# Kernel optimization log

Hardware: AMD Instinct MI355X
Metric: run time of the kernel (lower is better)

The kernel has to match this reference:

```python
import jax, jax.numpy as jnp
import numpy as np

N = 3072        # nodes
F_IN = 512      # input_dim
F_OUT = 256     # output_dim
ORDER = 2       # Cayley polynomial order
JACOBI = 3      # Jacobi fixed-point iterations per order


def setup_inputs() -> dict:
    key = jax.random.key(0)
    k1, k2, k3, k4, k5 = jax.random.split(key, 5)
    # normalized-adjacency-like matrix: row sums ~1 so h*Laplacian is well scaled
    adj = jax.random.uniform(k1, (N, N), dtype=jnp.float32) * (2.0 / N)
    x = jax.random.normal(k2, (N, F_IN), dtype=jnp.float32)
    h = jnp.float32(1.0)  # spectral zoom parameter
    w0 = jax.random.normal(k3, (F_IN, F_OUT), dtype=jnp.float32) * 0.05
    wr = jax.random.normal(k4, (ORDER, F_IN, F_OUT), dtype=jnp.float32) * 0.05
    wi = jax.random.normal(k5, (ORDER, F_IN, F_OUT), dtype=jnp.float32) * 0.05
    return {"x": x, "adj": adj, "h": h, "w0": w0, "wr": wr, "wi": wi}


def _cayley_forward(x, adj, h, w0, wr, wi):
    c64 = jnp.complex64
    j1 = jnp.asarray(1j, dtype=c64)
    n = adj.shape[0]
    I = jnp.eye(n, dtype=jnp.float32)
    # h * Laplacian, L = I - A_norm  (complex64, as in the TF code)
    hL = (h * (I - adj)).astype(c64)
    # Jacobi diagonal: rowsum(hL) + i  (constant across iterations)
    diag_inv = 1.0 / (jnp.sum(hL, axis=1) + j1)  # [n]

    # support[0] = I  ->  real part of I @ (x @ w0) is just x @ w0
    out = x @ w0  # [n, F_OUT] float32

    xc = x.astype(c64)
    csum = jnp.zeros((n, w0.shape[1]), dtype=c64)
    prev = I.astype(c64)
    for j in range(ORDER):
        # rhs of the linear system: x_j = hL @ prev - i*prev
        xj = hL @ prev - j1 * prev
        # Jacobi iterations: y <- y + D^{-1} (x_j - (hL @ y + i*y))
        y = xj
        for _ in range(JACOBI):
            y = y + diag_inv[:, None] * (xj - (hL @ y + j1 * y))
        W = jax.lax.complex(wr[j], wi[j])          # [F_IN, F_OUT] complex64
        csum = csum + y @ (xc @ W)                  # support_j @ pre_sup
        prev = y
    out = out + 2.0 * jnp.real(csum).astype(jnp.float32)
    return jax.nn.relu(out)


def reference(x, adj, h, w0, wr, wi):
    return _cayley_forward(x, adj, h, w0, wr, wi)
```

## Files before the change

kernel.cpp:

```cpp
#include <hip/hip_runtime.h>
#include <hip/hip_bf16.h>

#define NN 3072
#define FIN 512
#define FOUT 256

typedef __attribute__((ext_vector_type(8))) short short8;
typedef __attribute__((ext_vector_type(4))) float f32x4;

__device__ __forceinline__ short f2bf(float f) {
  union { float f; unsigned u; } v; v.f = f;
  unsigned r = v.u + 0x7fffu + ((v.u >> 16) & 1u);
  return (short)(r >> 16);
}

__device__ __forceinline__ void glds16(const short* g, short* l) {
  __builtin_amdgcn_global_load_lds(
      (const __attribute__((address_space(1))) unsigned*)g,
      (__attribute__((address_space(3))) unsigned*)l, 16, 0, 0);
}

template<int N> __device__ __forceinline__ void wait_vm() {
  if constexpr (N == 0) asm volatile("s_waitcnt vmcnt(0)" ::: "memory");
  else                  asm volatile("s_waitcnt vmcnt(4)" ::: "memory");
}


__global__ __launch_bounds__(256) void prep_adj(const float* __restrict__ adj,
    short* __restrict__ adjbf, float2* __restrict__ dinv, const float* __restrict__ hptr)
{
  int m = blockIdx.x;
  int tid = threadIdx.x;
  const float4* row = (const float4*)(adj + (size_t)m * NN);
  short4* obf = (short4*)(adjbf + (size_t)m * NN);
  float sum = 0.f;
#pragma unroll
  for (int i = 0; i < NN / 4 / 256; ++i) {
    int idx = i * 256 + tid;
    float4 v = row[idx];
    sum += (v.x + v.y) + (v.z + v.w);
    obf[idx] = make_short4(f2bf(v.x), f2bf(v.y), f2bf(v.z), f2bf(v.w));
  }
#pragma unroll
  for (int off = 32; off > 0; off >>= 1) sum += __shfl_down(sum, off, 64);
  __shared__ float red[4];
  if ((tid & 63) == 0) red[tid >> 6] = sum;
  __syncthreads();
  if (tid == 0) {
    float s = red[0] + red[1] + red[2] + red[3];
    float h = hptr[0];
    float r = h * (1.f - s);
    float den = r * r + 1.f;
    dinv[m] = make_float2(r / den, -1.f / den);
  }
}

__global__ __launch_bounds__(256) void prep_x(const float* __restrict__ x, short* __restrict__ xbf) {
  int idx = blockIdx.x * 256 + threadIdx.x;
  float4 v = ((const float4*)x)[idx];
  ((short4*)xbf)[idx] = make_short4(f2bf(v.x), f2bf(v.y), f2bf(v.z), f2bf(v.w));
}

__global__ __launch_bounds__(256) void prep_w(const float* __restrict__ w0,
    const float* __restrict__ wr, const float* __restrict__ wi, short* __restrict__ wpack)
{
  int idx = blockIdx.x * 256 + threadIdx.x;
  int f = idx & 511;
  int i = idx >> 9;
  float v;
  if (i < 1024) {
    int j = (i < 512) ? 1 : 0;
    int local = i & 511;
    int c = local >> 1;
    const float* src = (local & 1) ? wi : wr;
    v = src[((size_t)j * FIN + f) * FOUT + c];
  } else {
    v = w0[(size_t)f * FOUT + (i - 1024)];
  }
  wpack[idx] = f2bf(v);
}

template<int MODE, int KTOT, int ITILES>
__global__ __launch_bounds__(256, 4) void gemm_t(
    const short* __restrict__ Apan, int lda,
    const short* __restrict__ Badj, int ldb,
    const float* __restrict__ Vin,
    const float* __restrict__ Yin,
    float* __restrict__ Fout,
    short* __restrict__ Bout,
    const float2* __restrict__ dinv,
    const float* __restrict__ hptr)
{
  constexpr int BK = 64;
  constexpr int NT = KTOT / BK;

  __shared__ short As[2][64 * BK];
  __shared__ short Bs[2][64 * BK];

  const int tid  = threadIdx.x;
  const int lane = tid & 63;
  const int w    = tid >> 6;
  const int l15  = lane & 15;
  const int wrow = w >> 1, wcol = w & 1;

  const int bid = blockIdx.x;
  const int xcd = bid & 7;
  const int s   = bid >> 3;
  const int jt  = xcd * 6 + s / ITILES;
  const int it  = s % ITILES;

  const int i0 = it * 64;
  const int j0 = jt * 64;

  const int srow = lane >> 3;
  const int scol = ((lane & 7) ^ srow) * 8;

  const short* aSrc = Apan + (size_t)i0 * lda;
  const short* bSrc = Badj + (size_t)j0 * ldb;

  auto STAGE = [&](int t) {
    const int k0 = t * BK;
    short* at = As[t & 1];
    short* bt = Bs[t & 1];
#pragma unroll
    for (int li = 0; li < 2; ++li) {
      int rb = (w * 2 + li) * 8;
      glds16(aSrc + (size_t)(rb + srow) * lda + k0 + scol, at + rb * BK);
    }
#pragma unroll
    for (int li = 0; li < 2; ++li) {
      int rb = (w * 2 + li) * 8;
      glds16(bSrc + (size_t)(rb + srow) * ldb + k0 + scol, bt + rb * BK);
    }
  };

  f32x4 acc[2][2];
#pragma unroll
  for (int a = 0; a < 2; a++)
#pragma unroll
    for (int b = 0; b < 2; b++) acc[a][b] = (f32x4){0.f, 0.f, 0.f, 0.f};

  STAGE(0);
  STAGE(1);

  for (int t = 0; t < NT; ++t) {
    if (t < NT - 1) wait_vm<4>(); else wait_vm<0>();
    __builtin_amdgcn_s_barrier();
    asm volatile("" ::: "memory");

    const short* at = As[t & 1];
    const short* bt = Bs[t & 1];
#pragma unroll
    for (int kk = 0; kk < 2; ++kk) {
      const int cb = kk * 4 + (lane >> 4);
      short8 af[2], bfr[2];
#pragma unroll
      for (int a = 0; a < 2; ++a) {
        int ra = wrow * 32 + a * 16 + l15;
        int c = cb ^ (ra & 7);
        af[a] = *(const short8*)(at + ra * BK + c * 8);
      }
#pragma unroll
      for (int b = 0; b < 2; ++b) {
        int rb = wcol * 32 + b * 16 + l15;
        int c = cb ^ (rb & 7);
        bfr[b] = *(const short8*)(bt + rb * BK + c * 8);
      }
      __builtin_amdgcn_s_setprio(1);
#pragma unroll
      for (int a = 0; a < 2; ++a)
#pragma unroll
        for (int b = 0; b < 2; ++b)
          acc[a][b] = __builtin_amdgcn_mfma_f32_16x16x32_bf16(af[a], bfr[b], acc[a][b], 0, 0, 0);
      __builtin_amdgcn_s_setprio(0);
    }

    asm volatile("" ::: "memory");
    __builtin_amdgcn_s_barrier();
    asm volatile("" ::: "memory");
    if (t + 2 < NT) STAGE(t + 2);
  }

  const float hv = hptr[0];
  const int ibase = i0 + wrow * 32 + ((lane >> 4) << 2);
#pragma unroll
  for (int a = 0; a < 2; ++a) {
    const int ia = ibase + a * 16;
#pragma unroll
    for (int b = 0; b < 2; ++b) {
      const int jb = j0 + wcol * 32 + b * 16 + l15;
      f32x4 c = acc[a][b];
      if (MODE == 0) {
#pragma unroll
        for (int q = 0; q < 4; ++q) {
          size_t off = (size_t)(ia + q) * NN + jb;
          Fout[off] = c[q];
          if (ia + q < 1024) Bout[off] = f2bf(c[q]);
        }
      } else if (MODE == 1) {
#pragma unroll
        for (int p = 0; p < 4; p += 2) {
          size_t offr = (size_t)(ia + p) * NN + jb;
          size_t offi = offr + NN;
          float vr = Vin[offr], vi = Vin[offi];
          float outr = hv * (vr - c[p])     + vi;
          float outi = hv * (vi - c[p + 1]) - vr;
          Fout[offr] = outr; Fout[offi] = outi;
          Bout[offr] = f2bf(outr); Bout[offi] = f2bf(outi);
        }
      } else {
#pragma unroll
        for (int p = 0; p < 4; p += 2) {
          size_t offr = (size_t)(ia + p) * NN + jb;
          size_t offi = offr + NN;
          float2 dv = dinv[jb];
          float vr = Vin[offr], vi = Vin[offi];
          float yr = Yin[offr], yi = Yin[offi];
          float tr_ = hv * (yr - c[p])     - yi;
          float ti_ = hv * (yi - c[p + 1]) + yr;
          float er = vr - tr_, ei = vi - ti_;
          float nyr = yr + dv.x * er - dv.y * ei;
          float nyi = yi + dv.x * ei + dv.y * er;
          Fout[offr] = nyr; Fout[offi] = nyi;
          Bout[offr] = f2bf(nyr); Bout[offi] = f2bf(nyi);
        }
      }
    }
  }
}

__global__ __launch_bounds__(256) void final_out(
    const float* __restrict__ Vbuf,
    const float* __restrict__ ybuf,
    float* __restrict__ out)
{
  __shared__ float t[64][65];
  int n0 = blockIdx.x * 64;
  int c0 = blockIdx.y * 64;
  int lane = threadIdx.x & 63;
  int wv = threadIdx.x >> 6;
#pragma unroll
  for (int s = 0; s < 16; s++) {
    int c = c0 + wv + s * 4;
    float o0 = Vbuf[(size_t)(1024 + c) * NN + n0 + lane];
    float u  = ybuf[(size_t)(2 * c) * NN + n0 + lane];
    float sv = ybuf[(size_t)(512 + 2 * c) * NN + n0 + lane];
    float v = o0 + 2.f * (u + sv);
    t[lane][wv + s * 4] = v > 0.f ? v : 0.f;
  }
  __syncthreads();
#pragma unroll
  for (int s = 0; s < 16; s++) {
    int nl = wv + s * 4;
    out[(size_t)(n0 + nl) * FOUT + c0 + lane] = t[nl][lane];
  }
}

extern "C" void kernel_launch(void* const* d_in, const int* in_sizes, int n_in,
                              void* d_out, int out_size, void* d_ws, size_t ws_size,
                              hipStream_t stream) {
  const float* x   = (const float*)d_in[0];
  const float* adj = (const float*)d_in[1];
  const float* h   = (const float*)d_in[2];
  const float* w0  = (const float*)d_in[3];
  const float* wr  = (const float*)d_in[4];
  const float* wi  = (const float*)d_in[5];
  float* out = (float*)d_out;

  char* ws = (char*)d_ws;
  size_t off = 0;
  auto alloc = [&](size_t bytes) {
    char* p = ws + off;
    off += (bytes + 255) & ~(size_t)255;
    return p;
  };
  short*  adjbf = (short*)alloc((size_t)NN * NN * 2);
  short*  xbf   = (short*)alloc((size_t)NN * FIN * 2);
  short*  wpack = (short*)alloc((size_t)1280 * FIN * 2);
  float2* dinv  = (float2*)alloc((size_t)NN * sizeof(float2));
  float*  Vbuf  = (float*)alloc((size_t)1280 * NN * 4);
  float*  ybuf  = (float*)alloc((size_t)1024 * NN * 4);
  short*  b0    = (short*)alloc((size_t)1024 * NN * 2);
  short*  b1    = (short*)alloc((size_t)1024 * NN * 2);

  prep_adj<<<NN, 256, 0, stream>>>(adj, adjbf, dinv, h);
  prep_x<<<(NN * FIN / 4) / 256, 256, 0, stream>>>(x, xbf);
  prep_w<<<(1280 * FIN) / 256, 256, 0, stream>>>(w0, wr, wi, wpack);

  gemm_t<0, FIN, 20><<<dim3(48 * 20), 256, 0, stream>>>(
      wpack, FIN, xbf, FIN, nullptr, nullptr, Vbuf, b0, dinv, h);
  gemm_t<1, NN, 16><<<dim3(48 * 16), 256, 0, stream>>>(
      b0, NN, adjbf, NN, Vbuf, nullptr, Vbuf, b1, dinv, h);
  gemm_t<2, NN, 16><<<dim3(48 * 16), 256, 0, stream>>>(
      b1, NN, adjbf, NN, Vbuf, Vbuf, ybuf, b0, dinv, h);
  gemm_t<2, NN, 16><<<dim3(48 * 16), 256, 0, stream>>>(
      b0, NN, adjbf, NN, Vbuf, ybuf, ybuf, b1, dinv, h);
  gemm_t<2, NN, 16><<<dim3(48 * 16), 256, 0, stream>>>(
      b1, NN, adjbf, NN, Vbuf, ybuf, ybuf, b0, dinv, h);
  gemm_t<1, NN, 8><<<dim3(48 * 8), 256, 0, stream>>>(
      b0, NN, adjbf, NN, ybuf, nullptr, Vbuf, b1, dinv, h);
  gemm_t<2, NN, 8><<<dim3(48 * 8), 256, 0, stream>>>(
      b1, NN, adjbf, NN, Vbuf, Vbuf, ybuf, b0, dinv, h);
  gemm_t<2, NN, 8><<<dim3(48 * 8), 256, 0, stream>>>(
      b0, NN, adjbf, NN, Vbuf, ybuf, ybuf, b1, dinv, h);
  gemm_t<2, NN, 8><<<dim3(48 * 8), 256, 0, stream>>>(
      b1, NN, adjbf, NN, Vbuf, ybuf, ybuf, b0, dinv, h);

  final_out<<<dim3(48, 4), 256, 0, stream>>>(Vbuf, ybuf, out);
}
```

Measured before the change: 381.9 us.

## Apply Horner-style nesting to share one propagation chain across both orders

Rewrites the two-order Cayley sum so that the order-1 and order-2 contributions flow through a single chain of adjacency products acting on 512 columns, instead of 1024 columns for the first four GEMMs. The last Jacobi step of the first stage adds the order-1 projected features (a new MODE 3 epilogue), and the second stage then carries the combined sum. This roughly halves the N-dimension width of the first four big GEMMs. It also merges the x and w conversion kernels into one launch. It relies on linearity of the Jacobi iterations, and the bf16 rounding now happens along a different path.

```diff
diff --git a/kernel.cpp b/kernel.cpp
--- a/kernel.cpp
+++ b/kernel.cpp
@@ -55,29 +55,31 @@
   }
 }
 
-__global__ __launch_bounds__(256) void prep_x(const float* __restrict__ x, short* __restrict__ xbf) {
-  int idx = blockIdx.x * 256 + threadIdx.x;
-  float4 v = ((const float4*)x)[idx];
-  ((short4*)xbf)[idx] = make_short4(f2bf(v.x), f2bf(v.y), f2bf(v.z), f2bf(v.w));
-}
-
-__global__ __launch_bounds__(256) void prep_w(const float* __restrict__ w0,
-    const float* __restrict__ wr, const float* __restrict__ wi, short* __restrict__ wpack)
+__global__ __launch_bounds__(256) void prep_xw(const float* __restrict__ x,
+    const float* __restrict__ w0, const float* __restrict__ wr,
+    const float* __restrict__ wi, short* __restrict__ xbf, short* __restrict__ wpack)
 {
-  int idx = blockIdx.x * 256 + threadIdx.x;
-  int f = idx & 511;
-  int i = idx >> 9;
-  float v;
-  if (i < 1024) {
-    int j = (i < 512) ? 1 : 0;
-    int local = i & 511;
-    int c = local >> 1;
-    const float* src = (local & 1) ? wi : wr;
-    v = src[((size_t)j * FIN + f) * FOUT + c];
+  int b = blockIdx.x;
+  if (b < 1536) {
+    int idx = b * 256 + threadIdx.x;
+    float4 v = ((const float4*)x)[idx];
+    ((short4*)xbf)[idx] = make_short4(f2bf(v.x), f2bf(v.y), f2bf(v.z), f2bf(v.w));
   } else {
-    v = w0[(size_t)f * FOUT + (i - 1024)];
-  }
-  wpack[idx] = f2bf(v);
+    int idx = (b - 1536) * 256 + threadIdx.x;
+    int f = idx & 511;
+    int i = idx >> 9;
+    float v;
+    if (i < 1024) {
+      int j = (i < 512) ? 1 : 0;
+      int local = i & 511;
+      int c = local >> 1;
+      const float* src = (local & 1) ? wi : wr;
+      v = src[((size_t)j * FIN + f) * FOUT + c];
+    } else {
+      v = w0[(size_t)f * FOUT + (i - 1024)];
+    }
+    wpack[idx] = f2bf(v);
+  }
 }
 
 template<int MODE, int KTOT, int ITILES>
@@ -86,6 +88,7 @@
     const short* __restrict__ Badj, int ldb,
     const float* __restrict__ Vin,
     const float* __restrict__ Yin,
+    const float* __restrict__ Min,
     float* __restrict__ Fout,
     short* __restrict__ Bout,
     const float2* __restrict__ dinv,
@@ -221,6 +224,10 @@
           float er = vr - tr_, ei = vi - ti_;
           float nyr = yr + dv.x * er - dv.y * ei;
           float nyi = yi + dv.x * ei + dv.y * er;
+          if (MODE == 3) {
+            nyr += Min[offr];
+            nyi += Min[offi];
+          }
           Fout[offr] = nyr; Fout[offi] = nyi;
           Bout[offr] = f2bf(nyr); Bout[offi] = f2bf(nyi);
         }
@@ -244,8 +251,7 @@
     int c = c0 + wv + s * 4;
     float o0 = Vbuf[(size_t)(1024 + c) * NN + n0 + lane];
     float u  = ybuf[(size_t)(2 * c) * NN + n0 + lane];
-    float sv = ybuf[(size_t)(512 + 2 * c) * NN + n0 + lane];
-    float v = o0 + 2.f * (u + sv);
+    float v = o0 + 2.f * u;
     t[lane][wv + s * 4] = v > 0.f ? v : 0.f;
   }
   __syncthreads();
@@ -279,32 +285,37 @@
   short*  wpack = (short*)alloc((size_t)1280 * FIN * 2);
   float2* dinv  = (float2*)alloc((size_t)NN * sizeof(float2));
   float*  Vbuf  = (float*)alloc((size_t)1280 * NN * 4);
-  float*  ybuf  = (float*)alloc((size_t)1024 * NN * 4);
+  float*  xjbuf = (float*)alloc((size_t)512 * NN * 4);
+  float*  ybuf  = (float*)alloc((size_t)512 * NN * 4);
   short*  b0    = (short*)alloc((size_t)1024 * NN * 2);
-  short*  b1    = (short*)alloc((size_t)1024 * NN * 2);
+  short*  b1    = (short*)alloc((size_t)512 * NN * 2);
+  short*  b2    = (short*)alloc((size_t)512 * NN * 2);
 
   prep_adj<<<NN, 256, 0, stream>>>(adj, adjbf, dinv, h);
-  prep_x<<<(NN * FIN / 4) / 256, 256, 0, stream>>>(x, xbf);
-  prep_w<<<(1280 * FIN) / 256, 256, 0, stream>>>(w0, wr, wi, wpack);
+  prep_xw<<<4096, 256, 0, stream>>>(x, w0, wr, wi, xbf, wpack);
+
+  const float* Q0f = Vbuf + (size_t)512 * NN;
 
   gemm_t<0, FIN, 20><<<dim3(48 * 20), 256, 0, stream>>>(
-      wpack, FIN, xbf, FIN, nullptr, nullptr, Vbuf, b0, dinv, h);
-  gemm_t<1, NN, 16><<<dim3(48 * 16), 256, 0, stream>>>(
-      b0, NN, adjbf, NN, Vbuf, nullptr, Vbuf, b1, dinv, h);
-  gemm_t<2, NN, 16><<<dim3(48 * 16), 256, 0, stream>>>(
-      b1, NN, adjbf, NN, Vbuf, Vbuf, ybuf, b0, dinv, h);
-  gemm_t<2, NN, 16><<<dim3(48 * 16), 256, 0, stream>>>(
-      b0, NN, adjbf, NN, Vbuf, ybuf, ybuf, b1, dinv, h);
-  gemm_t<2, NN, 16><<<dim3(48 * 16), 256, 0, stream>>>(
-      b1, NN, adjbf, NN, Vbuf, ybuf, ybuf, b0, dinv, h);
+      wpack, FIN, xbf, FIN, nullptr, nullptr, nullptr, Vbuf, b0, dinv, h);
+
   gemm_t<1, NN, 8><<<dim3(48 * 8), 256, 0, stream>>>(
-      b0, NN, adjbf, NN, ybuf, nullptr, Vbuf, b1, dinv, h);
-  gemm_t<2, NN, 8><<<dim3(48 * 8), 256, 0, stream>>>(
-      b1, NN, adjbf, NN, Vbuf, Vbuf, ybuf, b0, dinv, h);
-  gemm_t<2, NN, 8><<<dim3(48 * 8), 256, 0, stream>>>(
-      b0, NN, adjbf, NN, Vbuf, ybuf, ybuf, b1, dinv, h);
-  gemm_t<2, NN, 8><<<dim3(48 * 8), 256, 0, stream>>>(
-      b1, NN, adjbf, NN, Vbuf, ybuf, ybuf, b0, dinv, h);
+      b0, NN, adjbf, NN, Vbuf, nullptr, nullptr, xjbuf, b1, dinv, h);
+  gemm_t<2, NN, 8><<<dim3(48 * 8), 256, 0, stream>>>(
+      b1, NN, adjbf, NN, xjbuf, xjbuf, nullptr, ybuf, b2, dinv, h);
+  gemm_t<2, NN, 8><<<dim3(48 * 8), 256, 0, stream>>>(
+      b2, NN, adjbf, NN, xjbuf, ybuf, nullptr, ybuf, b1, dinv, h);
+  gemm_t<3, NN, 8><<<dim3(48 * 8), 256, 0, stream>>>(
+      b1, NN, adjbf, NN, xjbuf, ybuf, Q0f, xjbuf, b2, dinv, h);
+
+  gemm_t<1, NN, 8><<<dim3(48 * 8), 256, 0, stream>>>(
+      b2, NN, adjbf, NN, xjbuf, nullptr, nullptr, xjbuf, b1, dinv, h);
+  gemm_t<2, NN, 8><<<dim3(48 * 8), 256, 0, stream>>>(
+      b1, NN, adjbf, NN, xjbuf, xjbuf, nullptr, ybuf, b2, dinv, h);
+  gemm_t<2, NN, 8><<<dim3(48 * 8), 256, 0, stream>>>(
+      b2, NN, adjbf, NN, xjbuf, ybuf, nullptr, ybuf, b1, dinv, h);
+  gemm_t<2, NN, 8><<<dim3(48 * 8), 256, 0, stream>>>(
+      b1, NN, adjbf, NN, xjbuf, ybuf, nullptr, ybuf, b2, dinv, h);
 
   final_out<<<dim3(48, 4), 256, 0, stream>>>(Vbuf, ybuf, out);
 }
```

Measured after the change: 370.3 us. 3.0% less time.
